# Kernel optimization log

Hardware: AMD Instinct MI355X
Metric: run time of the kernel (lower is better)

## Reference

```python
import jax, jax.numpy as jnp
import numpy as np

B, L, D = 8, 512, 32      # batch, seq_len, hidden_size (input dim)
N = 64                     # features_nodes (attention neurons)
H = 64                     # interm_layer_size (LSTM hidden)


def setup_inputs() -> dict:
    key = jax.random.key(0)
    ks = jax.random.split(key, 12)
    s = lambda k, shape, fan: jax.random.normal(k, shape, jnp.float32) * (1.0 / np.sqrt(fan))
    return {
        "text": jax.random.normal(ks[0], (B, L, D), jnp.float32),
        # AttentionLSTM params
        "Wx_w": s(ks[1], (N, D), D),
        "Wx_b": jnp.zeros((N,), jnp.float32),
        "Wxhat_w": s(ks[2], (N, D), D),
        "Wxhat_b": jnp.zeros((N,), jnp.float32),
        "att_w": s(ks[3], (1, N), N),
        "att_b": jnp.zeros((1,), jnp.float32),
        # unidirectional LSTM params (PyTorch layout: gates i,f,g,o)
        "W_ih": s(ks[4], (4 * H, D), D),
        "W_hh": s(ks[5], (4 * H, H), H),
        "b_ih": jnp.zeros((4 * H,), jnp.float32),
        "b_hh": jnp.zeros((4 * H,), jnp.float32),
        # dense head
        "dense_w": s(ks[6], (2, H), H),
        "dense_b": jnp.zeros((2,), jnp.float32),
    }


def _forward(text, Wx_w, Wx_b, Wxhat_w, Wxhat_b, att_w, att_b,
             W_ih, W_hh, b_ih, b_hh, dense_w, dense_b):
    # --- AttentionLSTM ---
    Wx = text @ Wx_w.T + Wx_b          # [B,L,N]
    # Wthat[b,i,j,:] = text[b,j,:], so Linear(Wthat) == Wxhat broadcast over i
    Wxhat = text @ Wxhat_w.T + Wxhat_b  # [B,L,N]
    # tanh(Wxhat[b,j] + Wx[b,i]) -> [B,L,L,N]
    t = jnp.tanh(Wxhat[:, None, :, :] + Wx[:, :, None, :])
    A = jax.nn.sigmoid(jnp.einsum('bijn,n->bij', t, att_w[0]) + att_b[0])  # [B,L,L]
    Xatt = jnp.einsum('bij,bjd->bid', A, text)  # sum_j Wthat*A -> [B,L,D]

    # --- unidirectional LSTM (last hidden state only) ---
    h0 = jnp.zeros((text.shape[0], H), text.dtype)
    c0 = jnp.zeros((text.shape[0], H), text.dtype)

    def step(carry, x_t):
        h, c = carry
        gates = x_t @ W_ih.T + b_ih + h @ W_hh.T + b_hh  # [B,4H]
        i, f, g, o = jnp.split(gates, 4, axis=-1)
        c = jax.nn.sigmoid(f) * c + jax.nn.sigmoid(i) * jnp.tanh(g)
        h = jax.nn.sigmoid(o) * jnp.tanh(c)
        return (h, c), None

    (h_last, _), _ = jax.lax.scan(step, (h0, c0), jnp.swapaxes(Xatt, 0, 1))
    return h_last @ dense_w.T + dense_b  # [B,2]


def reference(text, Wx_w, Wx_b, Wxhat_w, Wxhat_b, att_w, att_b,
              W_ih, W_hh, b_ih, b_hh, dense_w, dense_b):
    return _forward(text, Wx_w, Wx_b, Wxhat_w, Wxhat_b, att_w, att_b,
                    W_ih, W_hh, b_ih, b_hh, dense_w, dense_b)
```

## Files before the change

kernel.cpp:

```cpp
#include <hip/hip_runtime.h>
#include <hip/hip_bf16.h>

#define Bb 8
#define Ll 512
#define Dd 32
#define Nn 64
#define Hh 64
#define G4 256

#define L2E  1.4426950408889634f
#define L2E2 2.8853900817779268f

typedef _Float16 h2_t __attribute__((ext_vector_type(2)));

__device__ __forceinline__ float fast_rcp(float x) { return __builtin_amdgcn_rcpf(x); }
__device__ __forceinline__ float fast_exp2(float x) { return __builtin_amdgcn_exp2f(x); }

__device__ __forceinline__ float sig2(float x) {
    return fast_rcp(1.f + fast_exp2(-L2E * x));
}
__device__ __forceinline__ float tanh2(float x) {
    return fmaf(2.f, fast_rcp(1.f + fast_exp2(-L2E2 * x)), -1.f);
}

__device__ __forceinline__ float fdot2(h2_t a, h2_t b, float c) {
#if __has_builtin(__builtin_amdgcn_fdot2)
    return __builtin_amdgcn_fdot2(a, b, c, false);
#else
    return c + (float)a[0] * (float)b[0] + (float)a[1] * (float)b[1];
#endif
}

template<int CTRL>
__device__ __forceinline__ float quad_dpp(float v) {
    return __int_as_float(__builtin_amdgcn_mov_dpp(__float_as_int(v), CTRL, 0xf, 0xf, true));
}
__device__ __forceinline__ float quad_sum(float v) {
    v += quad_dpp<0xB1>(v);
    v += quad_dpp<0x4E>(v);
    return v;
}

__global__ __launch_bounds__(256) void k_proj(
    const float* __restrict__ text,
    const float* __restrict__ Wx_w, const float* __restrict__ Wx_b,
    const float* __restrict__ Wxh_w, const float* __restrict__ Wxh_b,
    float* __restrict__ Ex, float* __restrict__ Eh) {
    int idx = blockIdx.x * 256 + threadIdx.x;
    int n = idx & 63;
    int bl = idx >> 6;
    const float4* tr = (const float4*)(text + bl * Dd);
    const float4* w1 = (const float4*)(Wx_w + n * Dd);
    const float4* w2 = (const float4*)(Wxh_w + n * Dd);
    float a0 = 0.f, a1 = 0.f;
#pragma unroll
    for (int q = 0; q < 8; ++q) {
        float4 t4 = tr[q]; float4 x4 = w1[q]; float4 y4 = w2[q];
        a0 += t4.x * x4.x + t4.y * x4.y + t4.z * x4.z + t4.w * x4.w;
        a1 += t4.x * y4.x + t4.y * y4.y + t4.z * y4.z + t4.w * y4.w;
    }
    Ex[idx] = fast_exp2(L2E2 * (a0 + Wx_b[n]));
    Eh[idx] = fast_exp2(L2E2 * (a1 + Wxh_b[n]));
}

__global__ __launch_bounds__(256) void k_attn(
    const float* __restrict__ text,
    const float* __restrict__ Ex, const float* __restrict__ Eh,
    const float* __restrict__ att_w, const float* __restrict__ att_b,
    const float* __restrict__ W_ih, const float* __restrict__ b_ih,
    const float* __restrict__ b_hh, float* __restrict__ Gx) {
    __shared__ float s_eh[64 * 66];
    __shared__ float s_text[32 * 66];
    __shared__ float2 s_fa[4 * 64];
    __shared__ float s_A[4 * 64];
    __shared__ __align__(16) float s_xatt[4][32];

    int tid = threadIdx.x;
    int bx = blockIdx.x;
    int b = bx >> 7;
    int i0 = (bx & 127) << 2;
    int w = tid >> 6, l = tid & 63;
    int i = i0 + w;

    s_fa[w * 64 + l] = make_float2(Ex[((b * Ll) + i) * Nn + l], att_w[l]);
    float ab = att_b[0];
    __syncthreads();

    float awsum = 0.f;
#pragma unroll
    for (int n = 0; n < 64; ++n) awsum += s_fa[w * 64 + n].y;
    float zc = awsum + ab;

    float xacc = 0.f;
    int d = l & 31, hf = l >> 5;

    for (int jt = 0; jt < 8; ++jt) {
        __syncthreads();
        {
            int n = tid & 63; int j4 = tid >> 6;
#pragma unroll
            for (int r = 0; r < 16; ++r) {
                int jl = j4 + r * 4;
                s_eh[jl * 66 + n] = Eh[((b * Ll) + jt * 64 + jl) * Nn + n];
            }
            int dd = tid & 31; int j8 = tid >> 5;
#pragma unroll
            for (int r = 0; r < 8; ++r) {
                int jl = j8 + r * 8;
                s_text[dd * 66 + jl] = text[((b * Ll) + jt * 64 + jl) * Dd + dd];
            }
        }
        __syncthreads();
        float S = 0.f;
        const float* ehrow = &s_eh[l * 66];
        const float2* farow = &s_fa[w * 64];
#pragma unroll
        for (int n = 0; n < 64; n += 2) {
            float2 E2 = *(const float2*)(ehrow + n);
            float4 fa2 = *(const float4*)(farow + n);
            float r0 = fast_rcp(fmaf(E2.x, fa2.x, 1.f));
            S = fmaf(fa2.y, r0, S);
            float r1 = fast_rcp(fmaf(E2.y, fa2.z, 1.f));
            S = fmaf(fa2.w, r1, S);
        }
        float A = fast_rcp(1.f + fast_exp2(-L2E * (zc - 2.f * S)));
        s_A[w * 64 + l] = A;
#pragma unroll
        for (int jj = 0; jj < 32; jj += 2) {
            int j = hf * 32 + jj;
            float2 A2 = *(const float2*)&s_A[w * 64 + j];
            float2 T2 = *(const float2*)&s_text[d * 66 + j];
            xacc = fmaf(A2.x, T2.x, fmaf(A2.y, T2.y, xacc));
        }
    }
    xacc += __shfl_xor(xacc, 32);
    if (l < 32) s_xatt[w][l] = xacc;
    __syncthreads();

    {
        int r0 = tid;
        const float4* wr = (const float4*)(W_ih + r0 * Dd);
        float4 wv[8];
#pragma unroll
        for (int q = 0; q < 8; ++q) wv[q] = wr[q];
        float bias = b_ih[r0] + b_hh[r0];
#pragma unroll
        for (int r = 0; r < 4; ++r) {
            const float4* xr = (const float4*)s_xatt[r];
            float acc = bias;
#pragma unroll
            for (int q = 0; q < 8; ++q) {
                float4 x4 = xr[q]; float4 w4 = wv[q];
                acc += x4.x * w4.x + x4.y * w4.y + x4.z * w4.z + x4.w * w4.w;
            }
            Gx[((b * Ll) + i0 + r) * G4 + r0] = acc;
        }
    }
}

__global__ __launch_bounds__(256) void k_lstm(
    const float* __restrict__ Gx, const float* __restrict__ W_hh,
    const float* __restrict__ dense_w, const float* __restrict__ dense_b,
    float* __restrict__ out) {
    __shared__ __align__(16) _Float16 s_h[2][64];
    int b = blockIdx.x;
    int tid = threadIdx.x;
    int w = tid >> 6, l = tid & 63;
    int p = l & 3;
    int u = w * 16 + (l >> 2);

    h2_t wreg[4][8];
#pragma unroll
    for (int g = 0; g < 4; ++g) {
        const float4* wp = (const float4*)(W_hh + (g * 64 + u) * 64 + p * 16);
#pragma unroll
        for (int q = 0; q < 4; ++q) {
            float4 v = wp[q];
            wreg[g][2 * q]     = h2_t{(_Float16)v.x, (_Float16)v.y};
            wreg[g][2 * q + 1] = h2_t{(_Float16)v.z, (_Float16)v.w};
        }
    }

    if (tid < 64) s_h[0][tid] = (_Float16)0.f;
    float c = 0.f;
    const float* gxb = Gx + (size_t)b * Ll * G4;
    int gidx = p * 64 + u;
    float gx_cur = gxb[gidx];
    float gx_n1  = gxb[G4 + gidx];
    __syncthreads();

    int buf = 0;
    for (int t = 0; t < Ll; ++t) {
        int t2 = (t + 2 < Ll) ? (t + 2) : (Ll - 1);
        float gx_n2 = gxb[(size_t)t2 * G4 + gidx];

        union { float4 f; h2_t h[4]; } u0, u1;
        u0.f = *(const float4*)(&s_h[buf][p * 16]);
        u1.f = *(const float4*)(&s_h[buf][p * 16 + 8]);

        float a0 = (p == 0) ? gx_cur : 0.f;
        float a1 = (p == 1) ? gx_cur : 0.f;
        float a2 = (p == 2) ? gx_cur : 0.f;
        float a3 = (p == 3) ? gx_cur : 0.f;
#pragma unroll
        for (int q = 0; q < 4; ++q) {
            a0 = fdot2(u0.h[q], wreg[0][q], a0);
            a1 = fdot2(u0.h[q], wreg[1][q], a1);
            a2 = fdot2(u0.h[q], wreg[2][q], a2);
            a3 = fdot2(u0.h[q], wreg[3][q], a3);
        }
#pragma unroll
        for (int q = 0; q < 4; ++q) {
            a0 = fdot2(u1.h[q], wreg[0][q + 4], a0);
            a1 = fdot2(u1.h[q], wreg[1][q + 4], a1);
            a2 = fdot2(u1.h[q], wreg[2][q + 4], a2);
            a3 = fdot2(u1.h[q], wreg[3][q + 4], a3);
        }
        float ti = quad_sum(a0);
        float tf = quad_sum(a1);
        float tg = quad_sum(a2);
        float to = quad_sum(a3);

        float gi = sig2(ti);
        float gf = sig2(tf);
        float gg = tanh2(tg);
        float go = sig2(to);
        c = fmaf(gf, c, gi * gg);
        float hh = go * tanh2(c);
        if (p == 0) s_h[buf ^ 1][u] = (_Float16)hh;
        __syncthreads();
        buf ^= 1;
        gx_cur = gx_n1;
        gx_n1 = gx_n2;
    }
    if (tid == 0) {
        float a0 = dense_b[0], a1 = dense_b[1];
        for (int uu = 0; uu < 64; ++uu) {
            float hv = (float)s_h[buf][uu];
            a0 += hv * dense_w[uu];
            a1 += hv * dense_w[64 + uu];
        }
        out[b * 2 + 0] = a0;
        out[b * 2 + 1] = a1;
    }
}

extern "C" void kernel_launch(void* const* d_in, const int* in_sizes, int n_in,
                              void* d_out, int out_size, void* d_ws, size_t ws_size,
                              hipStream_t stream) {
    const float* text    = (const float*)d_in[0];
    const float* Wx_w    = (const float*)d_in[1];
    const float* Wx_b    = (const float*)d_in[2];
    const float* Wxh_w   = (const float*)d_in[3];
    const float* Wxh_b   = (const float*)d_in[4];
    const float* att_w   = (const float*)d_in[5];
    const float* att_b   = (const float*)d_in[6];
    const float* W_ih    = (const float*)d_in[7];
    const float* W_hh    = (const float*)d_in[8];
    const float* b_ih    = (const float*)d_in[9];
    const float* b_hh    = (const float*)d_in[10];
    const float* dense_w = (const float*)d_in[11];
    const float* dense_b = (const float*)d_in[12];

    float* ws   = (float*)d_ws;
    float* Ex   = ws;
    float* Eh   = ws + 262144;
    float* Gx   = ws + 655360;
    float* out  = (float*)d_out;

    hipLaunchKernelGGL(k_proj, dim3((Bb * Ll * Nn) / 256), dim3(256), 0, stream,
                       text, Wx_w, Wx_b, Wxh_w, Wxh_b, Ex, Eh);
    hipLaunchKernelGGL(k_attn, dim3(Bb * (Ll / 4)), dim3(256), 0, stream,
                       text, Ex, Eh, att_w, att_b, W_ih, b_ih, b_hh, Gx);
    hipLaunchKernelGGL(k_lstm, dim3(Bb), dim3(256), 0, stream,
                       Gx, W_hh, dense_w, dense_b, out);
}
```

Baseline: 200.1 us.

## Process two batch sequences per LSTM block and fold gate scaling into weights

The LSTM kernel now runs two batch elements per block, interleaving their dot products to expose more instruction-level parallelism in the latency-bound serial recurrence, and launches half as many blocks. The sigmoid/tanh exp2 scale factors are pre-multiplied into W_hh (before fp16 conversion) and into Gx in the attention kernel, removing a multiply per gate per step. The attention kernel keeps att_w in registers instead of interleaving it in shared memory. Risks are fp16 range/precision changes from scaled weights and more register pressure.

```diff
diff --git a/kernel.cpp b/kernel.cpp
--- a/kernel.cpp
+++ b/kernel.cpp
@@ -15,13 +15,6 @@
 
 __device__ __forceinline__ float fast_rcp(float x) { return __builtin_amdgcn_rcpf(x); }
 __device__ __forceinline__ float fast_exp2(float x) { return __builtin_amdgcn_exp2f(x); }
-
-__device__ __forceinline__ float sig2(float x) {
-    return fast_rcp(1.f + fast_exp2(-L2E * x));
-}
-__device__ __forceinline__ float tanh2(float x) {
-    return fmaf(2.f, fast_rcp(1.f + fast_exp2(-L2E2 * x)), -1.f);
-}
 
 __device__ __forceinline__ float fdot2(h2_t a, h2_t b, float c) {
 #if __has_builtin(__builtin_amdgcn_fdot2)
@@ -71,7 +64,7 @@
     const float* __restrict__ b_hh, float* __restrict__ Gx) {
     __shared__ float s_eh[64 * 66];
     __shared__ float s_text[32 * 66];
-    __shared__ float2 s_fa[4 * 64];
+    __shared__ float s_f[4 * 64];
     __shared__ float s_A[4 * 64];
     __shared__ __align__(16) float s_xatt[4][32];
 
@@ -82,14 +75,23 @@
     int w = tid >> 6, l = tid & 63;
     int i = i0 + w;
 
-    s_fa[w * 64 + l] = make_float2(Ex[((b * Ll) + i) * Nn + l], att_w[l]);
-    float ab = att_b[0];
+    float r_aw[64];
+    {
+        const float4* ap = (const float4*)att_w;
+#pragma unroll
+        for (int q = 0; q < 16; ++q) {
+            float4 v = ap[q];
+            r_aw[4 * q]     = v.x; r_aw[4 * q + 1] = v.y;
+            r_aw[4 * q + 2] = v.z; r_aw[4 * q + 3] = v.w;
+        }
+    }
+    float awsum = 0.f;
+#pragma unroll
+    for (int n = 0; n < 64; ++n) awsum += r_aw[n];
+
+    s_f[w * 64 + l] = Ex[((b * Ll) + i) * Nn + l];
+    float zc = awsum + att_b[0];
     __syncthreads();
-
-    float awsum = 0.f;
-#pragma unroll
-    for (int n = 0; n < 64; ++n) awsum += s_fa[w * 64 + n].y;
-    float zc = awsum + ab;
 
     float xacc = 0.f;
     int d = l & 31, hf = l >> 5;
@@ -113,15 +115,15 @@
         __syncthreads();
         float S = 0.f;
         const float* ehrow = &s_eh[l * 66];
-        const float2* farow = &s_fa[w * 64];
+        const float* frow = &s_f[w * 64];
 #pragma unroll
         for (int n = 0; n < 64; n += 2) {
             float2 E2 = *(const float2*)(ehrow + n);
-            float4 fa2 = *(const float4*)(farow + n);
-            float r0 = fast_rcp(fmaf(E2.x, fa2.x, 1.f));
-            S = fmaf(fa2.y, r0, S);
-            float r1 = fast_rcp(fmaf(E2.y, fa2.z, 1.f));
-            S = fmaf(fa2.w, r1, S);
+            float2 F2 = *(const float2*)(frow + n);
+            float r0v = fast_rcp(fmaf(E2.x, F2.x, 1.f));
+            S = fmaf(r_aw[n], r0v, S);
+            float r1v = fast_rcp(fmaf(E2.y, F2.y, 1.f));
+            S = fmaf(r_aw[n + 1], r1v, S);
         }
         float A = fast_rcp(1.f + fast_exp2(-L2E * (zc - 2.f * S)));
         s_A[w * 64 + l] = A;
@@ -139,6 +141,7 @@
 
     {
         int r0 = tid;
+        float sc = ((r0 >> 6) == 2) ? -L2E2 : -L2E;
         const float4* wr = (const float4*)(W_ih + r0 * Dd);
         float4 wv[8];
 #pragma unroll
@@ -153,7 +156,7 @@
                 float4 x4 = xr[q]; float4 w4 = wv[q];
                 acc += x4.x * w4.x + x4.y * w4.y + x4.z * w4.z + x4.w * w4.w;
             }
-            Gx[((b * Ll) + i0 + r) * G4 + r0] = acc;
+            Gx[((b * Ll) + i0 + r) * G4 + r0] = sc * acc;
         }
     }
 }
@@ -162,8 +165,8 @@
     const float* __restrict__ Gx, const float* __restrict__ W_hh,
     const float* __restrict__ dense_w, const float* __restrict__ dense_b,
     float* __restrict__ out) {
-    __shared__ __align__(16) _Float16 s_h[2][64];
-    int b = blockIdx.x;
+    __shared__ __align__(16) _Float16 s_h[2][2][64];
+    int bA = blockIdx.x * 2, bB = bA + 1;
     int tid = threadIdx.x;
     int w = tid >> 6, l = tid & 63;
     int p = l & 3;
@@ -172,76 +175,107 @@
     h2_t wreg[4][8];
 #pragma unroll
     for (int g = 0; g < 4; ++g) {
+        float sc = (g == 2) ? -L2E2 : -L2E;
         const float4* wp = (const float4*)(W_hh + (g * 64 + u) * 64 + p * 16);
 #pragma unroll
         for (int q = 0; q < 4; ++q) {
             float4 v = wp[q];
-            wreg[g][2 * q]     = h2_t{(_Float16)v.x, (_Float16)v.y};
-            wreg[g][2 * q + 1] = h2_t{(_Float16)v.z, (_Float16)v.w};
-        }
-    }
-
-    if (tid < 64) s_h[0][tid] = (_Float16)0.f;
-    float c = 0.f;
-    const float* gxb = Gx + (size_t)b * Ll * G4;
+            wreg[g][2 * q]     = h2_t{(_Float16)(sc * v.x), (_Float16)(sc * v.y)};
+            wreg[g][2 * q + 1] = h2_t{(_Float16)(sc * v.z), (_Float16)(sc * v.w)};
+        }
+    }
+
+    if (tid < 64) { s_h[0][0][tid] = (_Float16)0.f; s_h[1][0][tid] = (_Float16)0.f; }
+    float cA = 0.f, cB = 0.f;
+    const float* gxA = Gx + (size_t)bA * Ll * G4;
+    const float* gxB = Gx + (size_t)bB * Ll * G4;
     int gidx = p * 64 + u;
-    float gx_cur = gxb[gidx];
-    float gx_n1  = gxb[G4 + gidx];
+    float gxa_c = gxA[gidx], gxa_1 = gxA[G4 + gidx];
+    float gxb_c = gxB[gidx], gxb_1 = gxB[G4 + gidx];
     __syncthreads();
 
     int buf = 0;
     for (int t = 0; t < Ll; ++t) {
         int t2 = (t + 2 < Ll) ? (t + 2) : (Ll - 1);
-        float gx_n2 = gxb[(size_t)t2 * G4 + gidx];
-
-        union { float4 f; h2_t h[4]; } u0, u1;
-        u0.f = *(const float4*)(&s_h[buf][p * 16]);
-        u1.f = *(const float4*)(&s_h[buf][p * 16 + 8]);
-
-        float a0 = (p == 0) ? gx_cur : 0.f;
-        float a1 = (p == 1) ? gx_cur : 0.f;
-        float a2 = (p == 2) ? gx_cur : 0.f;
-        float a3 = (p == 3) ? gx_cur : 0.f;
+        float gxa_2 = gxA[(size_t)t2 * G4 + gidx];
+        float gxb_2 = gxB[(size_t)t2 * G4 + gidx];
+
+        union HU { float4 f; h2_t h[4]; };
+        HU ha0, ha1, hb0, hb1;
+        ha0.f = *(const float4*)(&s_h[0][buf][p * 16]);
+        ha1.f = *(const float4*)(&s_h[0][buf][p * 16 + 8]);
+        hb0.f = *(const float4*)(&s_h[1][buf][p * 16]);
+        hb1.f = *(const float4*)(&s_h[1][buf][p * 16 + 8]);
+
+        float aA0 = (p == 0) ? gxa_c : 0.f;
+        float aA1 = (p == 1) ? gxa_c : 0.f;
+        float aA2 = (p == 2) ? gxa_c : 0.f;
+        float aA3 = (p == 3) ? gxa_c : 0.f;
+        float aB0 = (p == 0) ? gxb_c : 0.f;
+        float aB1 = (p == 1) ? gxb_c : 0.f;
+        float aB2 = (p == 2) ? gxb_c : 0.f;
+        float aB3 = (p == 3) ? gxb_c : 0.f;
 #pragma unroll
         for (int q = 0; q < 4; ++q) {
-            a0 = fdot2(u0.h[q], wreg[0][q], a0);
-            a1 = fdot2(u0.h[q], wreg[1][q], a1);
-            a2 = fdot2(u0.h[q], wreg[2][q], a2);
-            a3 = fdot2(u0.h[q], wreg[3][q], a3);
+            aA0 = fdot2(ha0.h[q], wreg[0][q], aA0);
+            aB0 = fdot2(hb0.h[q], wreg[0][q], aB0);
+            aA1 = fdot2(ha0.h[q], wreg[1][q], aA1);
+            aB1 = fdot2(hb0.h[q], wreg[1][q], aB1);
+            aA2 = fdot2(ha0.h[q], wreg[2][q], aA2);
+            aB2 = fdot2(hb0.h[q], wreg[2][q], aB2);
+            aA3 = fdot2(ha0.h[q], wreg[3][q], aA3);
+            aB3 = fdot2(hb0.h[q], wreg[3][q], aB3);
         }
 #pragma unroll
         for (int q = 0; q < 4; ++q) {
-            a0 = fdot2(u1.h[q], wreg[0][q + 4], a0);
-            a1 = fdot2(u1.h[q], wreg[1][q + 4], a1);
-            a2 = fdot2(u1.h[q], wreg[2][q + 4], a2);
-            a3 = fdot2(u1.h[q], wreg[3][q + 4], a3);
-        }
-        float ti = quad_sum(a0);
-        float tf = quad_sum(a1);
-        float tg = quad_sum(a2);
-        float to = quad_sum(a3);
-
-        float gi = sig2(ti);
-        float gf = sig2(tf);
-        float gg = tanh2(tg);
-        float go = sig2(to);
-        c = fmaf(gf, c, gi * gg);
-        float hh = go * tanh2(c);
-        if (p == 0) s_h[buf ^ 1][u] = (_Float16)hh;
+            aA0 = fdot2(ha1.h[q], wreg[0][q + 4], aA0);
+            aB0 = fdot2(hb1.h[q], wreg[0][q + 4], aB0);
+            aA1 = fdot2(ha1.h[q], wreg[1][q + 4], aA1);
+            aB1 = fdot2(hb1.h[q], wreg[1][q + 4], aB1);
+            aA2 = fdot2(ha1.h[q], wreg[2][q + 4], aA2);
+            aB2 = fdot2(hb1.h[q], wreg[2][q + 4], aB2);
+            aA3 = fdot2(ha1.h[q], wreg[3][q + 4], aA3);
+            aB3 = fdot2(hb1.h[q], wreg[3][q + 4], aB3);
+        }
+        float tiA = quad_sum(aA0), tiB = quad_sum(aB0);
+        float tfA = quad_sum(aA1), tfB = quad_sum(aB1);
+        float tgA = quad_sum(aA2), tgB = quad_sum(aB2);
+        float toA = quad_sum(aA3), toB = quad_sum(aB3);
+
+        float giA = fast_rcp(1.f + fast_exp2(tiA));
+        float giB = fast_rcp(1.f + fast_exp2(tiB));
+        float gfA = fast_rcp(1.f + fast_exp2(tfA));
+        float gfB = fast_rcp(1.f + fast_exp2(tfB));
+        float ggA = fmaf(2.f, fast_rcp(1.f + fast_exp2(tgA)), -1.f);
+        float ggB = fmaf(2.f, fast_rcp(1.f + fast_exp2(tgB)), -1.f);
+        float goA = fast_rcp(1.f + fast_exp2(toA));
+        float goB = fast_rcp(1.f + fast_exp2(toB));
+        cA = fmaf(gfA, cA, giA * ggA);
+        cB = fmaf(gfB, cB, giB * ggB);
+        float thA = fmaf(2.f, fast_rcp(1.f + fast_exp2(-L2E2 * cA)), -1.f);
+        float thB = fmaf(2.f, fast_rcp(1.f + fast_exp2(-L2E2 * cB)), -1.f);
+        float hA = goA * thA;
+        float hB = goB * thB;
+        if (p == 0) {
+            s_h[0][buf ^ 1][u] = (_Float16)hA;
+            s_h[1][buf ^ 1][u] = (_Float16)hB;
+        }
         __syncthreads();
         buf ^= 1;
-        gx_cur = gx_n1;
-        gx_n1 = gx_n2;
-    }
-    if (tid == 0) {
-        float a0 = dense_b[0], a1 = dense_b[1];
-        for (int uu = 0; uu < 64; ++uu) {
-            float hv = (float)s_h[buf][uu];
-            a0 += hv * dense_w[uu];
-            a1 += hv * dense_w[64 + uu];
-        }
-        out[b * 2 + 0] = a0;
-        out[b * 2 + 1] = a1;
+        gxa_c = gxa_1; gxa_1 = gxa_2;
+        gxb_c = gxb_1; gxb_1 = gxb_2;
+    }
+    if (tid < 2) {
+        float a = dense_b[tid];
+        for (int uu = 0; uu < 64; ++uu)
+            a += (float)s_h[0][buf][uu] * dense_w[tid * 64 + uu];
+        out[bA * 2 + tid] = a;
+    } else if (tid >= 64 && tid < 66) {
+        int o = tid - 64;
+        float a = dense_b[o];
+        for (int uu = 0; uu < 64; ++uu)
+            a += (float)s_h[1][buf][uu] * dense_w[o * 64 + uu];
+        out[bB * 2 + o] = a;
     }
 }
 
@@ -272,6 +306,6 @@
                        text, Wx_w, Wx_b, Wxh_w, Wxh_b, Ex, Eh);
     hipLaunchKernelGGL(k_attn, dim3(Bb * (Ll / 4)), dim3(256), 0, stream,
                        text, Ex, Eh, att_w, att_b, W_ih, b_ih, b_hh, Gx);
-    hipLaunchKernelGGL(k_lstm, dim3(Bb), dim3(256), 0, stream,
+    hipLaunchKernelGGL(k_lstm, dim3(Bb / 2), dim3(256), 0, stream,
                        Gx, W_hh, dense_w, dense_b, out);
 }
```

New measurement: 265.3 us. +32.6%, slower.
